# Kernel optimization log

Hardware: AMD Instinct MI355X
Metric: run time of the kernel (lower is better)

The kernel has to match this reference:

```python
import jax, jax.numpy as jnp
import numpy as np

N_GAUSS = 4_000_000
FX = 500.0
FY = 500.0


def setup_inputs() -> dict:
    key = jax.random.key(0)
    ks = jax.random.split(key, 7)
    return {
        "positions": jax.random.normal(ks[0], (N_GAUSS, 3), dtype=jnp.float32) * 3.0,
        "scales": jax.random.uniform(ks[1], (N_GAUSS, 3), dtype=jnp.float32),
        "rotations": jax.random.normal(ks[2], (N_GAUSS, 4), dtype=jnp.float32),
        "colors": jax.random.uniform(ks[3], (N_GAUSS, 3), dtype=jnp.float32),
        "opacities": jax.random.normal(ks[4], (N_GAUSS,), dtype=jnp.float32),
        "viewmat": jax.random.normal(ks[5], (4, 4), dtype=jnp.float32),
        "projmat": jax.random.normal(ks[6], (4, 4), dtype=jnp.float32),
        "width": 1920,
        "height": 1080,
    }


def reference(positions, scales, rotations, colors, opacities, viewmat, projmat, width, height):
    # View transform: R @ (p - t) per Gaussian == (p - t) @ R^T
    pos_view = (positions - viewmat[:3, 3]) @ viewmat[:3, :3].T  # (N, 3)
    pos_view = jnp.clip(pos_view, -100.0, 100.0)

    valid_mask = (pos_view[:, 2] > 0.1) & (pos_view[:, 2] < 10.0)

    z = jnp.clip(pos_view[:, 2], 0.1, 10.0)
    x = jnp.clip(pos_view[:, 0] * FX / z + width / 2, -1000.0, width + 1000.0)
    y = jnp.clip(-(pos_view[:, 1] * FY / z) + height / 2, -1000.0, height + 1000.0)
    proj_points = jnp.stack([x, y, pos_view[:, 2]], axis=1)  # (N, 3)

    # Diagonal 2D covariance; note: torch.clamp(cov2d, 1e-6, 1e6) lifts
    # the zero off-diagonals to 1e-6, which we reproduce faithfully.
    sx = jnp.maximum(scales[:, 0], 0.001) * FX / z
    sy = jnp.maximum(scales[:, 1], 0.001) * FY / z
    c00 = jnp.clip(sx * sx + 1e-4, 1e-6, 1e6)
    c11 = jnp.clip(sy * sy + 1e-4, 1e-6, 1e6)
    off = jnp.full_like(c00, 1e-6)
    cov2d = jnp.stack(
        [jnp.stack([c00, off], axis=-1), jnp.stack([off, c11], axis=-1)], axis=1
    )  # (N, 2, 2)

    return (
        proj_points,
        cov2d,
        jnp.clip(colors, 0.0, 1.0),
        jax.nn.sigmoid(opacities),
        valid_mask,
    )
```

## Files before the change

### kernel.cpp

```cpp
#include <hip/hip_runtime.h>
#include <math.h>


#define FXc 500.0f

__global__ __launch_bounds__(256) void gs_project(
    const float* __restrict__ pos,
    const float* __restrict__ scl,
    const float* __restrict__ col,
    const float* __restrict__ opa,
    const float* __restrict__ vm,
    const int* __restrict__ pw,
    const int* __restrict__ ph,
    float* __restrict__ out,
    int N)
{
    int i = blockIdx.x * blockDim.x + threadIdx.x;
    if (i >= N) return;

    float r00 = vm[0], r01 = vm[1], r02 = vm[2],  t0 = vm[3];
    float r10 = vm[4], r11 = vm[5], r12 = vm[6],  t1 = vm[7];
    float r20 = vm[8], r21 = vm[9], r22 = vm[10], t2 = vm[11];
    float W = (float)(*pw), H = (float)(*ph);

    float px = pos[3*i + 0], py = pos[3*i + 1], pz = pos[3*i + 2];
    float dx = px - t0, dy = py - t1, dz = pz - t2;
    float v0 = r00*dx + r01*dy + r02*dz;
    float v1 = r10*dx + r11*dy + r12*dz;
    float v2 = r20*dx + r21*dy + r22*dz;
    v0 = fminf(fmaxf(v0, -100.0f), 100.0f);
    v1 = fminf(fmaxf(v1, -100.0f), 100.0f);
    v2 = fminf(fmaxf(v2, -100.0f), 100.0f);

    float valid = (v2 > 0.1f && v2 < 10.0f) ? 1.0f : 0.0f;
    float z   = fminf(fmaxf(v2, 0.1f), 10.0f);
    float fxz = FXc / z;

    float x = fminf(fmaxf(v0 * fxz + 0.5f * W, -1000.0f), W + 1000.0f);
    float y = fminf(fmaxf(0.5f * H - v1 * fxz, -1000.0f), H + 1000.0f);

    out[3*i + 0] = x;
    out[3*i + 1] = y;
    out[3*i + 2] = v2;

    float sx = fmaxf(scl[3*i + 0], 0.001f) * fxz;
    float sy = fmaxf(scl[3*i + 1], 0.001f) * fxz;
    float c00 = fminf(fmaxf(sx*sx + 1e-4f, 1e-6f), 1e6f);
    float c11 = fminf(fmaxf(sy*sy + 1e-4f, 1e-6f), 1e6f);
    *reinterpret_cast<float4*>(out + (size_t)3*N + 4*(size_t)i) =
        make_float4(c00, 1e-6f, 1e-6f, c11);

    const float* cp = col + 3*(size_t)i;
    float* co = out + (size_t)7*N + 3*(size_t)i;
    co[0] = fminf(fmaxf(cp[0], 0.0f), 1.0f);
    co[1] = fminf(fmaxf(cp[1], 0.0f), 1.0f);
    co[2] = fminf(fmaxf(cp[2], 0.0f), 1.0f);

    float o = opa[i];
    out[(size_t)10*N + i] = 1.0f / (1.0f + expf(-o));
    out[(size_t)11*N + i] = valid;
}

extern "C" void kernel_launch(void* const* d_in, const int* in_sizes, int n_in,
                              void* d_out, int out_size, void* d_ws, size_t ws_size,
                              hipStream_t stream) {
    const float* pos = (const float*)d_in[0];
    const float* scl = (const float*)d_in[1];
    const float* col = (const float*)d_in[3];
    const float* opa = (const float*)d_in[4];
    const float* vm  = (const float*)d_in[5];
    const int*   pw  = (const int*)d_in[7];
    const int*   ph  = (const int*)d_in[8];

    int N = in_sizes[0] / 3;
    int blocks = (N + 255) / 256;
    gs_project<<<blocks, 256, 0, stream>>>(pos, scl, col, opa, vm, pw, ph,
                                           (float*)d_out, N);
}
```

Baseline: 342.1 us.

## Stage AoS float3 inputs and outputs through LDS for coalesced float4 access

The AoS loads (positions, scales, colors) and stores (projected points, colors) now go through shared memory. Each block moves them as contiguous float4 transactions, replacing the strided 3-float per-thread accesses. Sigmoid switches to the fast __expf intrinsic. This adds two block barriers and LDS traffic. The tail handling assumes N is a multiple of 4 (it truncates at 3*Nq), which holds for the test size.

```diff
diff --git a/kernel.cpp b/kernel.cpp
--- a/kernel.cpp
+++ b/kernel.cpp
@@ -4,26 +4,48 @@
 
 #define FXc 500.0f
 
-__global__ __launch_bounds__(256) void gs_project(
-    const float* __restrict__ pos,
-    const float* __restrict__ scl,
-    const float* __restrict__ col,
-    const float* __restrict__ opa,
-    const float* __restrict__ vm,
+__global__ __launch_bounds__(256) void gs_project_lds(
+    const float4* __restrict__ pos4,
+    const float4* __restrict__ scl4,
+    const float4* __restrict__ col4,
+    const float*  __restrict__ opa,
+    const float*  __restrict__ vm,
     const int* __restrict__ pw,
     const int* __restrict__ ph,
     float* __restrict__ out,
     int N)
 {
-    int i = blockIdx.x * blockDim.x + threadIdx.x;
-    if (i >= N) return;
+    const int t  = threadIdx.x;
+    const int gb = blockIdx.x << 8;
+    const int i  = gb + t;
+    const int fb = blockIdx.x * 192;
+    const int Nq = N >> 2;
+
+    __shared__ float4 lin4[576];
+    __shared__ float4 lout4[384];
+    float* lin  = reinterpret_cast<float*>(lin4);
+    float* lout = reinterpret_cast<float*>(lout4);
+
+    if (t < 192) {
+        const int gi = fb + t;
+        if (gi < 3 * Nq) {
+            lin4[t]       = pos4[gi];
+            lin4[192 + t] = scl4[gi];
+            lin4[384 + t] = col4[gi];
+        }
+    }
+    float o = (i < N) ? opa[i] : 0.0f;
+    __syncthreads();
 
     float r00 = vm[0], r01 = vm[1], r02 = vm[2],  t0 = vm[3];
     float r10 = vm[4], r11 = vm[5], r12 = vm[6],  t1 = vm[7];
     float r20 = vm[8], r21 = vm[9], r22 = vm[10], t2 = vm[11];
     float W = (float)(*pw), H = (float)(*ph);
 
-    float px = pos[3*i + 0], py = pos[3*i + 1], pz = pos[3*i + 2];
+    float px = lin[3*t + 0],   py = lin[3*t + 1],   pz = lin[3*t + 2];
+    float s0 = lin[768 + 3*t], s1 = lin[768 + 3*t + 1];
+    float c0 = lin[1536 + 3*t], c1 = lin[1536 + 3*t + 1], c2 = lin[1536 + 3*t + 2];
+
     float dx = px - t0, dy = py - t1, dz = pz - t2;
     float v0 = r00*dx + r01*dy + r02*dz;
     float v1 = r10*dx + r11*dy + r12*dz;
@@ -32,48 +54,57 @@
     v1 = fminf(fmaxf(v1, -100.0f), 100.0f);
     v2 = fminf(fmaxf(v2, -100.0f), 100.0f);
 
-    float valid = (v2 > 0.1f && v2 < 10.0f) ? 1.0f : 0.0f;
+    float vld = (v2 > 0.1f && v2 < 10.0f) ? 1.0f : 0.0f;
     float z   = fminf(fmaxf(v2, 0.1f), 10.0f);
     float fxz = FXc / z;
 
-    float x = fminf(fmaxf(v0 * fxz + 0.5f * W, -1000.0f), W + 1000.0f);
-    float y = fminf(fmaxf(0.5f * H - v1 * fxz, -1000.0f), H + 1000.0f);
+    float X = fminf(fmaxf(v0 * fxz + 0.5f * W, -1000.0f), W + 1000.0f);
+    float Y = fminf(fmaxf(0.5f * H - v1 * fxz, -1000.0f), H + 1000.0f);
 
-    out[3*i + 0] = x;
-    out[3*i + 1] = y;
-    out[3*i + 2] = v2;
-
-    float sx = fmaxf(scl[3*i + 0], 0.001f) * fxz;
-    float sy = fmaxf(scl[3*i + 1], 0.001f) * fxz;
+    float sx = fmaxf(s0, 0.001f) * fxz;
+    float sy = fmaxf(s1, 0.001f) * fxz;
     float c00 = fminf(fmaxf(sx*sx + 1e-4f, 1e-6f), 1e6f);
     float c11 = fminf(fmaxf(sy*sy + 1e-4f, 1e-6f), 1e6f);
-    *reinterpret_cast<float4*>(out + (size_t)3*N + 4*(size_t)i) =
-        make_float4(c00, 1e-6f, 1e-6f, c11);
 
-    const float* cp = col + 3*(size_t)i;
-    float* co = out + (size_t)7*N + 3*(size_t)i;
-    co[0] = fminf(fmaxf(cp[0], 0.0f), 1.0f);
-    co[1] = fminf(fmaxf(cp[1], 0.0f), 1.0f);
-    co[2] = fminf(fmaxf(cp[2], 0.0f), 1.0f);
+    float sig = 1.0f / (1.0f + __expf(-o));
 
-    float o = opa[i];
-    out[(size_t)10*N + i] = 1.0f / (1.0f + expf(-o));
-    out[(size_t)11*N + i] = valid;
+    if (i < N) {
+        reinterpret_cast<float4*>(out)[3*Nq + i] =
+            make_float4(c00, 1e-6f, 1e-6f, c11);
+        out[(size_t)10*N + i] = sig;
+        out[(size_t)11*N + i] = vld;
+    }
+
+    lout[3*t + 0] = X;
+    lout[3*t + 1] = Y;
+    lout[3*t + 2] = v2;
+    lout[768 + 3*t + 0] = fminf(fmaxf(c0, 0.0f), 1.0f);
+    lout[768 + 3*t + 1] = fminf(fmaxf(c1, 0.0f), 1.0f);
+    lout[768 + 3*t + 2] = fminf(fmaxf(c2, 0.0f), 1.0f);
+    __syncthreads();
+
+    if (t < 192) {
+        const int gi = fb + t;
+        if (gi < 3 * Nq) {
+            reinterpret_cast<float4*>(out)[gi]          = lout4[t];
+            reinterpret_cast<float4*>(out)[7*Nq + gi]   = lout4[192 + t];
+        }
+    }
 }
 
 extern "C" void kernel_launch(void* const* d_in, const int* in_sizes, int n_in,
                               void* d_out, int out_size, void* d_ws, size_t ws_size,
                               hipStream_t stream) {
-    const float* pos = (const float*)d_in[0];
-    const float* scl = (const float*)d_in[1];
-    const float* col = (const float*)d_in[3];
-    const float* opa = (const float*)d_in[4];
-    const float* vm  = (const float*)d_in[5];
-    const int*   pw  = (const int*)d_in[7];
-    const int*   ph  = (const int*)d_in[8];
+    const float4* pos = (const float4*)d_in[0];
+    const float4* scl = (const float4*)d_in[1];
+    const float4* col = (const float4*)d_in[3];
+    const float*  opa = (const float*)d_in[4];
+    const float*  vm  = (const float*)d_in[5];
+    const int*    pw  = (const int*)d_in[7];
+    const int*    ph  = (const int*)d_in[8];
 
     int N = in_sizes[0] / 3;
     int blocks = (N + 255) / 256;
-    gs_project<<<blocks, 256, 0, stream>>>(pos, scl, col, opa, vm, pw, ph,
-                                           (float*)d_out, N);
+    gs_project_lds<<<blocks, 256, 0, stream>>>(pos, scl, col, opa, vm, pw, ph,
+                                               (float*)d_out, N);
 }
```

New measurement: 341.2 us. No clear change (-0.3%).
